# Optimization experiments

Hardware: AMD Instinct MI355X
Metric: run time of the kernel (lower is better)

Reference implementation:

```python
import jax, jax.numpy as jnp
import numpy as np

N_NODES = 200000
N_EDGES = 3200000
N_FEAT = 8
DT_INIT = 0.3
DT_MIN, DT_MAX = 0.02, 2.0
CG_MAX_ITER = 30
CG_TOL = 1e-4
G_INIT = 9.81


def setup_inputs() -> dict:
    key = jax.random.key(0)
    k1, k2, k3, k4 = jax.random.split(key, 4)
    u_now = jax.random.normal(k1, (N_NODES, N_FEAT), dtype=jnp.float32)
    # DAG edges: src < dst (required by the module's topo-level build)
    a = jax.random.randint(k2, (N_EDGES,), 0, N_NODES)
    b = jax.random.randint(k3, (N_EDGES,), 0, N_NODES)
    src = jnp.minimum(a, b)
    dst = jnp.maximum(a, b)
    dst = jnp.where(src == dst, jnp.minimum(dst + 1, N_NODES - 1), dst)
    src = jnp.where(src == dst, jnp.maximum(src - 1, 0), src)
    edge_index = jnp.stack([src, dst]).astype(jnp.int64)
    # edge_attr[:,0]=dx (positive), edge_attr[:,1]=dz
    edge_attr = jax.random.uniform(k4, (N_EDGES, 2), dtype=jnp.float32,
                                   minval=0.05, maxval=1.0)
    dt = jnp.asarray(DT_INIT, dtype=jnp.float32)
    g_hat = jnp.asarray(G_INIT, dtype=jnp.float32)
    return {"u_now": u_now, "edge_index": edge_index, "edge_attr": edge_attr,
            "dt": dt, "g_hat": g_hat}


def _cg_solve(mv, rhs, max_iter, tol):
    # matches torch cg_solve with x0=None (zeros)
    x = jnp.zeros_like(rhs)
    r = rhs - mv(x)
    p = r
    rs = jnp.sum(r * r)

    def body(i, state):
        x, r, p, rs, done = state
        Ap = mv(p)
        alpha = rs / (jnp.sum(p * Ap) + 1e-12)
        x1 = x + alpha * p
        r1 = r - alpha * Ap
        rs1 = jnp.sum(r1 * r1)
        done1 = done | (jnp.sqrt(rs1) <= tol)
        beta = rs1 / (rs + 1e-12)
        p1 = r1 + beta * p
        sel = lambda old, new: jnp.where(done, old, new)
        return (sel(x, x1), sel(r, r1), sel(p, p1),
                jnp.where(done, rs, rs1), done1)

    x, _, _, _, _ = jax.lax.fori_loop(
        0, max_iter, body, (x, r, p, rs, jnp.array(False)))
    return x


def reference(u_now, edge_index, edge_attr, dt, g_hat):
    src, dst = edge_index[0], edge_index[1]
    E = src.shape[0]
    F = u_now.shape[1]
    dx = jnp.clip(edge_attr[:, 0], 1e-6, None)        # [E]
    inv = (1.0 / dx)[:, None]                         # [E,1]
    slope_e = (edge_attr[:, 1] / dx)[:, None]         # [E,1] dz/dx
    dt_eff = jnp.clip(dt, DT_MIN, DT_MAX)

    def D1(x):  # upwind: out[i] += (x[i]-x[j])*inv_dx
        return jnp.zeros_like(x).at[dst].add((x[dst] - x[src]) * inv)

    def D1_T(y):
        yd = y[dst] * inv
        return jnp.zeros_like(y).at[dst].add(yd).at[src].add(-yd)

    A_mv = lambda v: v + dt_eff * (u_now * D1(v))
    AT_mv = lambda y: y + dt_eff * D1_T(u_now * y)

    # slope source term scattered to dst nodes
    slope_n = jnp.zeros_like(u_now).at[dst].add(
        jnp.broadcast_to(slope_e, (E, F)))
    b = u_now - dt_eff * g_hat * slope_n

    # necg: solve (A^T A) x = A^T b via CG
    rhs = AT_mv(b)
    mv = lambda v: AT_mv(A_mv(v))
    u_next = _cg_solve(mv, rhs, CG_MAX_ITER, CG_TOL)
    return u_next
```

## Files before the change

kernel.cpp:

```cpp
#include <hip/hip_runtime.h>
#include <math.h>
#include <stdint.h>
#include <string.h>


#define F 8
#define CG_ITERS 30
#define LEAF_T 4096
#define LEAF_PAD (LEAF_T + LEAF_T / 128 + 8)
#define ENC_ADD 1024
#define MAX_LEAF 1024
#define MAX_CLS 32


#define LV(A_, i_) A_[(i_) + ((i_) >> 7)]

struct __align__(8) Ed { int n; float v; };
struct __align__(16) Rec { int e; int n; float v; float s; };

struct Sched {
    int NL, uNT, uMaxD, nCls;
    int leafOff[MAX_LEAF], leafN[MAX_LEAF], cls[MAX_LEAF];
    int cNB[MAX_CLS], cMaxD[MAX_CLS];
    int cBOff[MAX_CLS][64], cBN[MAX_CLS][64];
    int cA[MAX_CLS][64], cB[MAX_CLS][64], cOrder[MAX_CLS][64];
    int cLevOff[MAX_CLS][32];
    int uA[MAX_LEAF], uB[MAX_LEAF], uOrder[MAX_LEAF], uLevOff[64];
};


static void host_build_tree(int n, int T, int* bOff, int* bN,
                            int* A, int* B, int* dep,
                            int* pNB, int* pNT, int* pMaxD) {
    int so[64], sn[64], st[64], sid[64], sdp[64];
    int sp = 0, coff = 0, cn = n, c2 = 0, t = 0, rootd = 0;
    for (;;) {
        if (cn <= T) {
            if (bOff) { bOff[c2] = coff; bN[c2] = cn; }
            int id = c2, dp = 0; c2++;
            bool fin = false;
            for (;;) {
                if (sp == 0) { rootd = dp; fin = true; break; }
                if (st[sp - 1] == 0) {
                    st[sp - 1] = 1; sid[sp - 1] = id; sdp[sp - 1] = dp;
                    int n2 = sn[sp - 1] / 2; n2 -= (n2 & 7);
                    coff = so[sp - 1] + n2; cn = sn[sp - 1] - n2;
                    break;
                } else {
                    A[t] = sid[sp - 1]; B[t] = id;
                    int dA = sdp[sp - 1];
                    dp = ((dA > dp) ? dA : dp) + 1;
                    dep[t] = dp;
                    id = ENC_ADD + t; t++;
                    sp--;
                }
            }
            if (fin) break;
        } else {
            so[sp] = coff; sn[sp] = cn; st[sp] = 0; sp++;
            int n2 = cn / 2; n2 -= (n2 & 7);
            cn = n2;
        }
    }
    *pNB = c2; *pNT = t; *pMaxD = rootd;
}

static void host_bucketize(const int* dep, int NT, int maxD,
                           int* order, int* levOff) {
    int cnt[64];
    for (int d = 0; d <= maxD; ++d) cnt[d] = 0;
    for (int t = 0; t < NT; ++t) cnt[dep[t]]++;
    int run = 0;
    levOff[0] = 0;
    for (int d = 1; d <= maxD; ++d) { run += cnt[d]; levOff[d] = run; }
    int cur[64];
    for (int d = 1; d <= maxD; ++d) cur[d] = levOff[d - 1];
    for (int t = 0; t < NT; ++t) { int d = dep[t]; order[cur[d]++] = t; }
}

static void build_sched_host(int n, Sched* s) {
    static int uDep[MAX_LEAF];
    host_build_tree(n, LEAF_T, s->leafOff, s->leafN, s->uA, s->uB, uDep,
                    &s->NL, &s->uNT, &s->uMaxD);
    host_bucketize(uDep, s->uNT, s->uMaxD, s->uOrder, s->uLevOff);
    s->nCls = 0;
    int clsN[MAX_CLS];
    int dep[64];
    for (int j = 0; j < s->NL; ++j) {
        int c = -1;
        for (int k = 0; k < s->nCls; ++k)
            if (clsN[k] == s->leafN[j]) { c = k; break; }
        if (c < 0 && s->nCls < MAX_CLS) {
            c = s->nCls++;
            clsN[c] = s->leafN[j];
            int NB, NT, maxD;
            host_build_tree(s->leafN[j], 128, s->cBOff[c], s->cBN[c],
                            s->cA[c], s->cB[c], dep, &NB, &NT, &maxD);
            s->cNB[c] = NB; s->cMaxD[c] = maxD;
            host_bucketize(dep, NT, maxD, s->cOrder[c], s->cLevOff[c]);
        }
        s->cls[j] = c;
    }
}


__device__ __forceinline__ float dt_eff_of(const float* dtp) {
    return fminf(fmaxf(dtp[0], 0.02f), 2.0f);
}

__device__ __forceinline__ int slotOf(int e, int NB) {
    return (e < ENC_ADD) ? e : (NB + (e - ENC_ADD));
}

__device__ __forceinline__ float combine_upper(const float* __restrict__ partial,
                                               const Sched* __restrict__ sc,
                                               float* sU, int lane) {
    int NL = sc->NL, NT = sc->uNT, maxD = sc->uMaxD;
    for (int k = lane; k < NL; k += 256) sU[k] = partial[k];
    __syncthreads();
    for (int d = 1; d <= maxD; ++d) {
        int s0 = sc->uLevOff[d - 1], s1 = sc->uLevOff[d];
        for (int s = s0 + lane; s < s1; s += 256) {
            int tt = sc->uOrder[s];
            sU[NL + tt] = __fadd_rn(sU[slotOf(sc->uA[tt], NL)],
                                    sU[slotOf(sc->uB[tt], NL)]);
        }
        __syncthreads();
    }
    return (NT > 0) ? sU[NL + NT - 1] : sU[0];
}

__device__ __forceinline__ void dot_eval(const float* sA, const float* sB,
                                         float* sChain, float* sVal,
                                         int lane, int NB,
                                         const int* __restrict__ bOff,
                                         const int* __restrict__ bN,
                                         const int* __restrict__ A,
                                         const int* __restrict__ Bb,
                                         const int* __restrict__ order,
                                         const int* __restrict__ levOff,
                                         int maxD,
                                         float* __restrict__ partial, int j) {
    int bb = lane >> 3, jj = lane & 7;
    if (bb < NB) {
        int off = bOff[bb], n = bN[bb];
        if (n >= 8) {
            int lim = n - (n & 7);
            float rr = __fmul_rn(LV(sA, off + jj), LV(sB, off + jj));
            for (int e = jj + 8; e < lim; e += 8)
                rr = __fadd_rn(rr, __fmul_rn(LV(sA, off + e), LV(sB, off + e)));
            sChain[bb * 8 + jj] = rr;
        }
    }
    __syncthreads();
    if (lane < NB) {
        int off = bOff[lane], n = bN[lane];
        float res;
        if (n < 8) {
            res = 0.f;
            for (int e = 0; e < n; ++e)
                res = __fadd_rn(res, __fmul_rn(LV(sA, off + e), LV(sB, off + e)));
        } else {
            int lim = n - (n & 7);
            const float* c = sChain + lane * 8;
            res = __fadd_rn(__fadd_rn(__fadd_rn(c[0], c[1]), __fadd_rn(c[2], c[3])),
                            __fadd_rn(__fadd_rn(c[4], c[5]), __fadd_rn(c[6], c[7])));
            for (int e = lim; e < n; ++e)
                res = __fadd_rn(res, __fmul_rn(LV(sA, off + e), LV(sB, off + e)));
        }
        sVal[lane] = res;
    }
    __syncthreads();
    for (int d = 1; d <= maxD; ++d) {
        int s0 = levOff[d - 1], s1 = levOff[d];
        for (int s = s0 + lane; s < s1; s += 256) {
            int tt = order[s];
            sVal[NB + tt] = __fadd_rn(sVal[slotOf(A[tt], NB)],
                                      sVal[slotOf(Bb[tt], NB)]);
        }
        __syncthreads();
    }
    if (lane == 0) partial[j] = (NB > 1) ? sVal[NB + NB - 2] : sVal[0];
}

__global__ void k_dot_leaf(const float* __restrict__ a, const float* __restrict__ b,
                           const Sched* __restrict__ sc, float* __restrict__ partial) {
    __shared__ float sA[LEAF_PAD], sB[LEAF_PAD];
    __shared__ float sChain[512];
    __shared__ float sVal[160];
    int j = blockIdx.x, lane = threadIdx.x;
    int P = sc->leafOff[j] + 1, nn = sc->leafN[j];
    for (int g = lane; g < nn; g += 256) {
        float av = a[P + g], bv = b[P + g];
        int m = g + (g >> 7);
        sA[m] = av; sB[m] = bv;
    }
    __syncthreads();
    int c = sc->cls[j];
    dot_eval(sA, sB, sChain, sVal, lane, sc->cNB[c], sc->cBOff[c], sc->cBN[c],
             sc->cA[c], sc->cB[c], sc->cOrder[c], sc->cLevOff[c], sc->cMaxD[c],
             partial, j);
}

__global__ void k_dot_rs0(const float* __restrict__ a,
                          const float* __restrict__ partial,
                          const Sched* __restrict__ sc, float* __restrict__ scal) {
    __shared__ float sU[2048];
    int lane = threadIdx.x;
    float res = combine_upper(partial, sc, sU, lane);
    if (lane == 0)
        scal[8 + 0] = __fadd_rn(__fmul_rn(a[0], a[0]), res);
}

__global__ void k_xr_dot(float* __restrict__ x, float* __restrict__ r,
                         const float* __restrict__ p, const float* __restrict__ z,
                         const float* __restrict__ scal,
                         const Sched* __restrict__ sc,
                         const float* __restrict__ partial1,
                         float* __restrict__ partial2, int it) {
    __shared__ float sA[LEAF_PAD];
    __shared__ float sU[2048];
    __shared__ float sChain[512];
    __shared__ float sVal[160];
    __shared__ float sAl;
    __shared__ int   sAct;
    int j = blockIdx.x, lane = threadIdx.x;
    float res = combine_upper(partial1, sc, sU, lane);
    if (lane == 0) {
        float pt = __fadd_rn(__fmul_rn(p[0], z[0]), res);
        sAl = __fdiv_rn(scal[8 + it], __fadd_rn(pt, (float)1e-12));
        sAct = (scal[64 + it] == 0.f) ? 1 : 0;
    }
    __syncthreads();
    int active = sAct;
    float al = sAl;
    int P = sc->leafOff[j] + 1, nn = sc->leafN[j];
    if (j == 0 && lane == 0 && active) {
        x[0] = __fadd_rn(x[0], __fmul_rn(al, p[0]));
        r[0] = __fsub_rn(r[0], __fmul_rn(al, z[0]));
    }
    for (int g = lane; g < nn; g += 256) {
        int q = P + g;
        float rv = r[q];
        if (active) {
            float xv = x[q], pv = p[q], zv = z[q];
            x[q] = __fadd_rn(xv, __fmul_rn(al, pv));
            rv = __fsub_rn(rv, __fmul_rn(al, zv));
            r[q] = rv;
        }
        sA[g + (g >> 7)] = rv;
    }
    __syncthreads();
    int c = sc->cls[j];
    dot_eval(sA, sA, sChain, sVal, lane, sc->cNB[c], sc->cBOff[c], sc->cBN[c],
             sc->cA[c], sc->cB[c], sc->cOrder[c], sc->cLevOff[c], sc->cMaxD[c],
             partial2, j);
}

__global__ void k_p_fin(float4* __restrict__ p4, const float4* __restrict__ r4,
                        const float* __restrict__ rfull,
                        float* __restrict__ scal,
                        const Sched* __restrict__ sc,
                        const float* __restrict__ partial2, int it, int n4) {
    __shared__ float sU[2048];
    __shared__ float sBe;
    __shared__ int   sAct;
    int lane = threadIdx.x;
    float res = combine_upper(partial2, sc, sU, lane);
    if (lane == 0) {
        float rs1 = __fadd_rn(__fmul_rn(rfull[0], rfull[0]), res);
        float RS = scal[8 + it];
        float dn = scal[64 + it];
        sBe = __fdiv_rn(rs1, __fadd_rn(RS, (float)1e-12));
        sAct = (dn == 0.f) ? 1 : 0;
        if (blockIdx.x == 0) {
            scal[8 + it + 1]  = (dn == 0.f) ? rs1 : RS;
            scal[64 + it + 1] = (dn != 0.f || __fsqrt_rn(rs1) <= (float)1e-4)
                                ? 1.f : 0.f;
        }
    }
    __syncthreads();
    if (!sAct) return;
    float be = sBe;
    int i = blockIdx.x * blockDim.x + lane;
    if (i >= n4) return;
    float4 pv = p4[i], rv = r4[i];
    pv.x = __fadd_rn(rv.x, __fmul_rn(be, pv.x));
    pv.y = __fadd_rn(rv.y, __fmul_rn(be, pv.y));
    pv.z = __fadd_rn(rv.z, __fmul_rn(be, pv.z));
    pv.w = __fadd_rn(rv.w, __fmul_rn(be, pv.w));
    p4[i] = pv;
}


__global__ void k_edge_pre(const int* __restrict__ dst, const int* __restrict__ src,
                           int* __restrict__ dstCnt, int* __restrict__ srcCnt, int E) {
    int e = blockIdx.x * blockDim.x + threadIdx.x;
    if (e >= E) return;
    atomicAdd(&dstCnt[dst[e]], 1);
    atomicAdd(&srcCnt[src[e]], 1);
}

__global__ void k_scan1(const int* __restrict__ cnt, int* __restrict__ incl,
                        int* __restrict__ bsums, int N) {
    __shared__ int sm[512];
    int i = blockIdx.x * 512 + threadIdx.x;
    sm[threadIdx.x] = (i < N) ? cnt[i] : 0;
    __syncthreads();
    for (int off = 1; off < 512; off <<= 1) {
        int t = (threadIdx.x >= off) ? sm[threadIdx.x - off] : 0;
        __syncthreads();
        sm[threadIdx.x] += t;
        __syncthreads();
    }
    if (i < N) incl[i] = sm[threadIdx.x];
    if (threadIdx.x == 511) bsums[blockIdx.x] = sm[511];
}

__global__ void k_scan2(int* __restrict__ bsums, int nb) {
    __shared__ int sm[512];
    sm[threadIdx.x] = (threadIdx.x < nb) ? bsums[threadIdx.x] : 0;
    __syncthreads();
    for (int off = 1; off < 512; off <<= 1) {
        int t = (threadIdx.x >= off) ? sm[threadIdx.x - off] : 0;
        __syncthreads();
        sm[threadIdx.x] += t;
        __syncthreads();
    }
    if (threadIdx.x < nb) bsums[threadIdx.x] = sm[threadIdx.x];
}

__global__ void k_scan3(int* __restrict__ off, const int* __restrict__ bsums,
                        const int* __restrict__ cnt, int N, int E) {
    int i = blockIdx.x * 512 + threadIdx.x;
    if (i < N) {
        int add = (blockIdx.x > 0) ? bsums[blockIdx.x - 1] : 0;
        off[i] = off[i] + add - cnt[i];
    }
    if (i == 0) off[N] = E;
}

__global__ void k_fill(const int* __restrict__ dst, const int* __restrict__ src,
                       const float* __restrict__ ea,
                       const int* __restrict__ dstOff, const int* __restrict__ srcOff,
                       int* __restrict__ cursD, int* __restrict__ cursS,
                       Rec* __restrict__ recD, Rec* __restrict__ recS, int E) {
    int e = blockIdx.x * blockDim.x + threadIdx.x;
    if (e >= E) return;
    int d = dst[e];
    int s0 = src[e];
    float2 exy = ((const float2*)ea)[e];
    float dx = fmaxf(exy.x, 1e-6f);
    float iv = __fdiv_rn(1.f, dx);
    float sl = __fdiv_rn(exy.y, dx);
    Rec rd; rd.e = e; rd.n = s0; rd.v = iv; rd.s = sl;
    Rec rs; rs.e = e; rs.n = d;  rs.v = iv; rs.s = 0.f;
    recD[dstOff[d] + atomicAdd(&cursD[d], 1)] = rd;
    recS[srcOff[s0] + atomicAdd(&cursS[s0], 1)] = rs;
}

__device__ __forceinline__ void insortR(Rec* L, int lo, int hi) {
    for (int a = lo + 1; a < hi; ++a) {
        Rec key = L[a]; int b = a - 1;
        while (b >= lo && L[b].e > key.e) { L[b + 1] = L[b]; b--; }
        L[b + 1] = key;
    }
}

__global__ void k_sort(const int* __restrict__ dstOff, const int* __restrict__ srcOff,
                       Rec* __restrict__ recD, Rec* __restrict__ recS, int N) {
    int i = blockIdx.x * blockDim.x + threadIdx.x;
    if (i >= N) return;
    insortR(recD, dstOff[i], dstOff[i + 1]);
    insortR(recS, srcOff[i], srcOff[i + 1]);
}

__global__ void k_compact(const Rec* __restrict__ recD, const Rec* __restrict__ recS,
                          Ed* __restrict__ edD, float* __restrict__ slopeD,
                          Ed* __restrict__ edS, int E) {
    int k = blockIdx.x * blockDim.x + threadIdx.x;
    if (k >= E) return;
    Rec rd = recD[k];
    Rec rs = recS[k];
    Ed d0; d0.n = rd.n; d0.v = rd.v;
    Ed s0; s0.n = rs.n; s0.v = rs.v;
    edD[k] = d0;
    edS[k] = s0;
    slopeD[k] = rd.s;
}


__global__ void k_slope_b(const float* __restrict__ u, const float* __restrict__ slopeD,
                          const int* __restrict__ dstOff,
                          float* __restrict__ r, float* __restrict__ y,
                          const float* __restrict__ dtp, const float* __restrict__ gp,
                          int N) {
    int i = blockIdx.x * blockDim.x + threadIdx.x;
    if (i >= N) return;
    float dtg = __fmul_rn(dt_eff_of(dtp), gp[0]);
    float sn = 0.f;
    int k0 = dstOff[i], k1 = dstOff[i + 1];
    for (int k = k0; k < k1; ++k) sn = __fadd_rn(sn, slopeD[k]);
    float ms = __fmul_rn(dtg, sn);
    const float4* u4 = (const float4*)u;
    float4* r4 = (float4*)r;
    float4* y4 = (float4*)y;
    #pragma unroll
    for (int hh = 0; hh < 2; ++hh) {
        float4 uv = u4[i * 2 + hh];
        float4 bv;
        bv.x = __fsub_rn(uv.x, ms);
        bv.y = __fsub_rn(uv.y, ms);
        bv.z = __fsub_rn(uv.z, ms);
        bv.w = __fsub_rn(uv.w, ms);
        r4[i * 2 + hh] = bv;
        float4 yv;
        yv.x = __fmul_rn(uv.x, bv.x);
        yv.y = __fmul_rn(uv.y, bv.y);
        yv.z = __fmul_rn(uv.z, bv.z);
        yv.w = __fmul_rn(uv.w, bv.w);
        y4[i * 2 + hh] = yv;
    }
}

__global__ void k_d1tz_full(const Ed* __restrict__ edD, const int* __restrict__ dstOff,
                            const Ed* __restrict__ edS, const int* __restrict__ srcOff,
                            const float* __restrict__ y,
                            const float* __restrict__ base, float* __restrict__ out,
                            const float* __restrict__ dtp,
                            float* __restrict__ rInit, float* __restrict__ xInit,
                            int NP) {
    int idx = blockIdx.x * blockDim.x + threadIdx.x;
    if (idx >= NP) return;
    int i = idx >> 2, c = idx & 3;
    const float2* y2 = (const float2*)y;
    float2 uy = y2[idx];
    float2 acc = make_float2(0.f, 0.f);
    int k0 = dstOff[i], k1 = dstOff[i + 1];
    #pragma unroll 4
    for (int k = k0; k < k1; ++k) {
        float iv = edD[k].v;
        acc.x = __fadd_rn(acc.x, __fmul_rn(uy.x, iv));
        acc.y = __fadd_rn(acc.y, __fmul_rn(uy.y, iv));
    }
    k0 = srcOff[i]; k1 = srcOff[i + 1];
    #pragma unroll 4
    for (int k = k0; k < k1; ++k) {
        Ed e = edS[k];
        float2 yd = y2[e.n * 4 + c];
        float t0 = __fmul_rn(yd.x, e.v); acc.x = __fadd_rn(acc.x, -t0);
        float t1 = __fmul_rn(yd.y, e.v); acc.y = __fadd_rn(acc.y, -t1);
    }
    float dt = dt_eff_of(dtp);
    float2 bs = ((const float2*)base)[idx];
    float2 ov;
    ov.x = __fadd_rn(bs.x, __fmul_rn(dt, acc.x));
    ov.y = __fadd_rn(bs.y, __fmul_rn(dt, acc.y));
    ((float2*)out)[idx] = ov;
    ((float2*)rInit)[idx] = ov;
    ((float2*)xInit)[idx] = make_float2(0.f, 0.f);
}

__global__ void k_d1w_f(const Ed* __restrict__ edD, const int* __restrict__ dstOff,
                        const float* __restrict__ pv, const float* __restrict__ u,
                        float* __restrict__ w, float* __restrict__ y,
                        float* __restrict__ dacc,
                        const float* __restrict__ dtp, int NP) {
    int idx = blockIdx.x * blockDim.x + threadIdx.x;
    if (idx >= NP) return;
    int i = idx >> 2, c = idx & 3;
    const float2* pv2 = (const float2*)pv;
    float2 pi = pv2[idx];
    float2 acc = make_float2(0.f, 0.f);
    int k0 = dstOff[i], k1 = dstOff[i + 1];
    #pragma unroll 4
    for (int k = k0; k < k1; ++k) {
        Ed e = edD[k];
        float2 ps = pv2[e.n * 4 + c];
        acc.x = __fadd_rn(acc.x, __fmul_rn(__fsub_rn(pi.x, ps.x), e.v));
        acc.y = __fadd_rn(acc.y, __fmul_rn(__fsub_rn(pi.y, ps.y), e.v));
    }
    float dt = dt_eff_of(dtp);
    float2 uv = ((const float2*)u)[idx];
    float2 wv;
    wv.x = __fadd_rn(pi.x, __fmul_rn(dt, __fmul_rn(uv.x, acc.x)));
    wv.y = __fadd_rn(pi.y, __fmul_rn(dt, __fmul_rn(uv.y, acc.y)));
    ((float2*)w)[idx] = wv;
    float2 yv;
    yv.x = __fmul_rn(uv.x, wv.x);
    yv.y = __fmul_rn(uv.y, wv.y);
    ((float2*)y)[idx] = yv;
    float2 da = make_float2(0.f, 0.f);
    #pragma unroll 4
    for (int k = k0; k < k1; ++k) {
        float iv = edD[k].v;
        da.x = __fadd_rn(da.x, __fmul_rn(yv.x, iv));
        da.y = __fadd_rn(da.y, __fmul_rn(yv.y, iv));
    }
    ((float2*)dacc)[idx] = da;
}

__global__ void k_d1tzs(const Ed* __restrict__ edS, const int* __restrict__ srcOff,
                        const float* __restrict__ y, const float* __restrict__ dacc,
                        const float* __restrict__ base, float* __restrict__ out,
                        const float* __restrict__ dtp, int NP) {
    int idx = blockIdx.x * blockDim.x + threadIdx.x;
    if (idx >= NP) return;
    int i = idx >> 2, c = idx & 3;
    const float2* y2 = (const float2*)y;
    float2 acc = ((const float2*)dacc)[idx];
    int k0 = srcOff[i], k1 = srcOff[i + 1];
    #pragma unroll 4
    for (int k = k0; k < k1; ++k) {
        Ed e = edS[k];
        float2 yd = y2[e.n * 4 + c];
        float t0 = __fmul_rn(yd.x, e.v); acc.x = __fadd_rn(acc.x, -t0);
        float t1 = __fmul_rn(yd.y, e.v); acc.y = __fadd_rn(acc.y, -t1);
    }
    float dt = dt_eff_of(dtp);
    float2 bs = ((const float2*)base)[idx];
    float2 ov;
    ov.x = __fadd_rn(bs.x, __fmul_rn(dt, acc.x));
    ov.y = __fadd_rn(bs.y, __fmul_rn(dt, acc.y));
    ((float2*)out)[idx] = ov;
}

extern "C" void kernel_launch(void* const* d_in, const int* in_sizes, int n_in,
                              void* d_out, int out_size, void* d_ws, size_t ws_size,
                              hipStream_t stream) {
    const float* u   = (const float*)d_in[0];
    const int*   ei  = (const int*)d_in[1];
    const float* ea  = (const float*)d_in[2];
    const float* dtp = (const float*)d_in[3];
    const float* gp  = (const float*)d_in[4];

    const int NF = in_sizes[0];
    const int N  = NF / F;
    const int E  = in_sizes[2] / 2;
    const int* srcp = ei;
    const int* dstp = ei + E;

    static Sched h_sched;
    build_sched_host(NF - 1, &h_sched);
    const int NL = h_sched.NL;

    char* wp = (char*)d_ws;
    float* scal    = (float*)wp; wp += 128 * 4;
    float* r       = (float*)wp; wp += (size_t)NF * 4;
    float* p       = (float*)wp; wp += (size_t)NF * 4;
    float* t       = (float*)wp; wp += (size_t)NF * 4;
    float* w       = (float*)wp; wp += (size_t)NF * 4;
    float* y       = (float*)wp; wp += (size_t)NF * 4;
    float* dacc    = (float*)wp; wp += (size_t)NF * 4;
    Rec*   recD    = (Rec*)wp;   wp += (size_t)E * 16;
    Rec*   recS    = (Rec*)wp;   wp += (size_t)E * 16;
    Ed*    edD     = (Ed*)wp;    wp += (size_t)E * 8;
    Ed*    edS     = (Ed*)wp;    wp += (size_t)E * 8;
    float* slopeD  = (float*)wp; wp += (size_t)E * 4;
    int*   dstOff  = (int*)wp;   wp += (size_t)(N + 1) * 4;
    int*   srcOff  = (int*)wp;   wp += (size_t)(N + 1) * 4;
    int*   dstCnt  = (int*)wp;   wp += (size_t)N * 4;
    int*   srcCnt  = (int*)wp;   wp += (size_t)N * 4;
    int*   cursD   = (int*)wp;   wp += (size_t)N * 4;
    int*   cursS   = (int*)wp;   wp += (size_t)N * 4;
    int*   bsD     = (int*)wp;   wp += 512 * 4;
    int*   bsS     = (int*)wp;   wp += 512 * 4;
    float* partial1 = (float*)wp; wp += 2048 * 4;
    float* partial2 = (float*)wp; wp += 2048 * 4;
    wp = (char*)(((uintptr_t)wp + 255) & ~(uintptr_t)255);
    Sched* d_sched = (Sched*)wp; wp += (sizeof(Sched) + 255) & ~(size_t)255;
    float* x = (float*)d_out;

    hipMemcpyAsync(d_sched, &h_sched, sizeof(Sched), hipMemcpyHostToDevice,
                   stream);
    hipMemsetAsync(scal, 0, 128 * 4, stream);
    hipMemsetAsync(dstCnt, 0, (size_t)N * 4, stream);
    hipMemsetAsync(srcCnt, 0, (size_t)N * 4, stream);
    hipMemsetAsync(cursD, 0, (size_t)N * 4, stream);
    hipMemsetAsync(cursS, 0, (size_t)N * 4, stream);

    const int bn = 256;
    const int gN  = (N + bn - 1) / bn;
    const int gE  = (E + bn - 1) / bn;
    const int nb  = (N + 511) / 512;
    const int n4  = NF / 4;
    const int g4  = (n4 + bn - 1) / bn;
    const int NP  = NF / 2;
    const int gP  = (NP + bn - 1) / bn;

    k_edge_pre<<<gE, bn, 0, stream>>>(dstp, srcp, dstCnt, srcCnt, E);
    k_scan1<<<nb, 512, 0, stream>>>(dstCnt, dstOff, bsD, N);
    k_scan2<<<1, 512, 0, stream>>>(bsD, nb);
    k_scan3<<<nb, 512, 0, stream>>>(dstOff, bsD, dstCnt, N, E);
    k_scan1<<<nb, 512, 0, stream>>>(srcCnt, srcOff, bsS, N);
    k_scan2<<<1, 512, 0, stream>>>(bsS, nb);
    k_scan3<<<nb, 512, 0, stream>>>(srcOff, bsS, srcCnt, N, E);
    k_fill<<<gE, bn, 0, stream>>>(dstp, srcp, ea, dstOff, srcOff, cursD, cursS,
                                  recD, recS, E);
    k_sort<<<gN, bn, 0, stream>>>(dstOff, srcOff, recD, recS, N);
    k_compact<<<gE, bn, 0, stream>>>(recD, recS, edD, slopeD, edS, E);

    k_slope_b<<<gN, bn, 0, stream>>>(u, slopeD, dstOff, r, y, dtp, gp, N);
    k_d1tz_full<<<gP, bn, 0, stream>>>(edD, dstOff, edS, srcOff,
                                       y, r, p, dtp, r, x, NP);
    k_dot_leaf<<<NL, 256, 0, stream>>>(p, p, d_sched, partial1);
    k_dot_rs0<<<1, 256, 0, stream>>>(p, partial1, d_sched, scal);

    for (int it = 0; it < CG_ITERS; ++it) {
        k_d1w_f<<<gP, bn, 0, stream>>>(edD, dstOff, p, u, w, y, dacc, dtp, NP);
        k_d1tzs<<<gP, bn, 0, stream>>>(edS, srcOff, y, dacc, w, t, dtp, NP);
        k_dot_leaf<<<NL, 256, 0, stream>>>(p, t, d_sched, partial1);
        k_xr_dot<<<NL, 256, 0, stream>>>(x, r, p, t, scal, d_sched,
                                         partial1, partial2, it);
        k_p_fin<<<g4, bn, 0, stream>>>((float4*)p, (const float4*)r, r, scal,
                                       d_sched, partial2, it, n4);
    }
}
```

Measured before the change: 4.662 ms.

## Fuse CSR scans, merge sort+compact with shared-memory key sort, merge memsets

Merges the dst and src prefix-scan kernels into combined launches, replaces the in-place global-memory insertion sort plus separate compact pass with a single kernel that sorts packed (edge id, local index) keys in shared memory and writes compacted edge arrays directly, and collapses four memsets into one contiguous memset. This is meant to cut launch count and the global-memory traffic of sorting 16-byte records in place. Shared memory of 64 KB per block may limit occupancy, and nodes with degree above 64 fall back to a quadratic selection scan. The single memset relies on dstCnt, srcCnt, cursD and cursS being contiguous in the workspace.

After: 4.568 ms. -2.0%, faster.

```diff
diff --git a/kernel.cpp b/kernel.cpp
--- a/kernel.cpp
+++ b/kernel.cpp
@@ -11,6 +11,7 @@
 #define ENC_ADD 1024
 #define MAX_LEAF 1024
 #define MAX_CLS 32
+#define MAXDEG 64
 
 
 #define LV(A_, i_) A_[(i_) + ((i_) >> 7)]
@@ -301,10 +302,18 @@
     atomicAdd(&srcCnt[src[e]], 1);
 }
 
-__global__ void k_scan1(const int* __restrict__ cnt, int* __restrict__ incl,
-                        int* __restrict__ bsums, int N) {
+__global__ void k_scan1m(const int* __restrict__ cntD, const int* __restrict__ cntS,
+                         int* __restrict__ inclD, int* __restrict__ inclS,
+                         int* __restrict__ bsD, int* __restrict__ bsS,
+                         int N, int nb) {
     __shared__ int sm[512];
-    int i = blockIdx.x * 512 + threadIdx.x;
+    int bb = blockIdx.x;
+    int isS = (bb >= nb) ? 1 : 0;
+    int blk = bb - (isS ? nb : 0);
+    const int* cnt = isS ? cntS : cntD;
+    int* incl = isS ? inclS : inclD;
+    int* bsums = isS ? bsS : bsD;
+    int i = blk * 512 + threadIdx.x;
     sm[threadIdx.x] = (i < N) ? cnt[i] : 0;
     __syncthreads();
     for (int off = 1; off < 512; off <<= 1) {
@@ -314,27 +323,39 @@
         __syncthreads();
     }
     if (i < N) incl[i] = sm[threadIdx.x];
-    if (threadIdx.x == 511) bsums[blockIdx.x] = sm[511];
-}
-
-__global__ void k_scan2(int* __restrict__ bsums, int nb) {
+    if (threadIdx.x == 511) bsums[blk] = sm[511];
+}
+
+__global__ void k_scan2m(int* __restrict__ bsD, int* __restrict__ bsS, int nb) {
     __shared__ int sm[512];
-    sm[threadIdx.x] = (threadIdx.x < nb) ? bsums[threadIdx.x] : 0;
-    __syncthreads();
-    for (int off = 1; off < 512; off <<= 1) {
-        int t = (threadIdx.x >= off) ? sm[threadIdx.x - off] : 0;
+    for (int pass = 0; pass < 2; ++pass) {
+        int* bsums = pass ? bsS : bsD;
+        sm[threadIdx.x] = (threadIdx.x < nb) ? bsums[threadIdx.x] : 0;
         __syncthreads();
-        sm[threadIdx.x] += t;
+        for (int off = 1; off < 512; off <<= 1) {
+            int t = (threadIdx.x >= off) ? sm[threadIdx.x - off] : 0;
+            __syncthreads();
+            sm[threadIdx.x] += t;
+            __syncthreads();
+        }
+        if (threadIdx.x < nb) bsums[threadIdx.x] = sm[threadIdx.x];
         __syncthreads();
     }
-    if (threadIdx.x < nb) bsums[threadIdx.x] = sm[threadIdx.x];
-}
-
-__global__ void k_scan3(int* __restrict__ off, const int* __restrict__ bsums,
-                        const int* __restrict__ cnt, int N, int E) {
-    int i = blockIdx.x * 512 + threadIdx.x;
+}
+
+__global__ void k_scan3m(int* __restrict__ offD, int* __restrict__ offS,
+                         const int* __restrict__ bsD, const int* __restrict__ bsS,
+                         const int* __restrict__ cntD, const int* __restrict__ cntS,
+                         int N, int E, int nb) {
+    int bb = blockIdx.x;
+    int isS = (bb >= nb) ? 1 : 0;
+    int blk = bb - (isS ? nb : 0);
+    int* off = isS ? offS : offD;
+    const int* bsums = isS ? bsS : bsD;
+    const int* cnt = isS ? cntS : cntD;
+    int i = blk * 512 + threadIdx.x;
     if (i < N) {
-        int add = (blockIdx.x > 0) ? bsums[blockIdx.x - 1] : 0;
+        int add = (blk > 0) ? bsums[blk - 1] : 0;
         off[i] = off[i] + add - cnt[i];
     }
     if (i == 0) off[N] = E;
@@ -359,34 +380,74 @@
     recS[srcOff[s0] + atomicAdd(&cursS[s0], 1)] = rs;
 }
 
-__device__ __forceinline__ void insortR(Rec* L, int lo, int hi) {
-    for (int a = lo + 1; a < hi; ++a) {
-        Rec key = L[a]; int b = a - 1;
-        while (b >= lo && L[b].e > key.e) { L[b + 1] = L[b]; b--; }
-        L[b + 1] = key;
-    }
-}
-
-__global__ void k_sort(const int* __restrict__ dstOff, const int* __restrict__ srcOff,
-                       Rec* __restrict__ recD, Rec* __restrict__ recS, int N) {
+__global__ void k_sortc(const int* __restrict__ dstOff, const int* __restrict__ srcOff,
+                        const Rec* __restrict__ recD, const Rec* __restrict__ recS,
+                        Ed* __restrict__ edD, float* __restrict__ slopeD,
+                        Ed* __restrict__ edS, int N) {
+    __shared__ unsigned keys[256 * MAXDEG];
     int i = blockIdx.x * blockDim.x + threadIdx.x;
     if (i >= N) return;
-    insortR(recD, dstOff[i], dstOff[i + 1]);
-    insortR(recS, srcOff[i], srcOff[i + 1]);
-}
-
-__global__ void k_compact(const Rec* __restrict__ recD, const Rec* __restrict__ recS,
-                          Ed* __restrict__ edD, float* __restrict__ slopeD,
-                          Ed* __restrict__ edS, int E) {
-    int k = blockIdx.x * blockDim.x + threadIdx.x;
-    if (k >= E) return;
-    Rec rd = recD[k];
-    Rec rs = recS[k];
-    Ed d0; d0.n = rd.n; d0.v = rd.v;
-    Ed s0; s0.n = rs.n; s0.v = rs.v;
-    edD[k] = d0;
-    edS[k] = s0;
-    slopeD[k] = rd.s;
+    unsigned* k0 = keys + threadIdx.x * MAXDEG;
+    {
+        int lo = dstOff[i], hi = dstOff[i + 1], d = hi - lo;
+        if (d <= MAXDEG) {
+            for (int m = 0; m < d; ++m)
+                k0[m] = ((unsigned)recD[lo + m].e << 6) | (unsigned)m;
+            for (int a = 1; a < d; ++a) {
+                unsigned kk = k0[a]; int b = a - 1;
+                while (b >= 0 && k0[b] > kk) { k0[b + 1] = k0[b]; b--; }
+                k0[b + 1] = kk;
+            }
+            for (int m = 0; m < d; ++m) {
+                Rec rr = recD[lo + (int)(k0[m] & 63u)];
+                Ed ed; ed.n = rr.n; ed.v = rr.v;
+                edD[lo + m] = ed; slopeD[lo + m] = rr.s;
+            }
+        } else {
+            int prev = -1;
+            for (int m = 0; m < d; ++m) {
+                int best = 0x7fffffff, bj = -1;
+                for (int jx = 0; jx < d; ++jx) {
+                    int ev = recD[lo + jx].e;
+                    if (ev > prev && ev < best) { best = ev; bj = jx; }
+                }
+                Rec rr = recD[lo + bj];
+                Ed ed; ed.n = rr.n; ed.v = rr.v;
+                edD[lo + m] = ed; slopeD[lo + m] = rr.s;
+                prev = best;
+            }
+        }
+    }
+    {
+        int lo = srcOff[i], hi = srcOff[i + 1], d = hi - lo;
+        if (d <= MAXDEG) {
+            for (int m = 0; m < d; ++m)
+                k0[m] = ((unsigned)recS[lo + m].e << 6) | (unsigned)m;
+            for (int a = 1; a < d; ++a) {
+                unsigned kk = k0[a]; int b = a - 1;
+                while (b >= 0 && k0[b] > kk) { k0[b + 1] = k0[b]; b--; }
+                k0[b + 1] = kk;
+            }
+            for (int m = 0; m < d; ++m) {
+                Rec rr = recS[lo + (int)(k0[m] & 63u)];
+                Ed ed; ed.n = rr.n; ed.v = rr.v;
+                edS[lo + m] = ed;
+            }
+        } else {
+            int prev = -1;
+            for (int m = 0; m < d; ++m) {
+                int best = 0x7fffffff, bj = -1;
+                for (int jx = 0; jx < d; ++jx) {
+                    int ev = recS[lo + jx].e;
+                    if (ev > prev && ev < best) { best = ev; bj = jx; }
+                }
+                Rec rr = recS[lo + bj];
+                Ed ed; ed.n = rr.n; ed.v = rr.v;
+                edS[lo + m] = ed;
+                prev = best;
+            }
+        }
+    }
 }
 
 
@@ -574,10 +635,7 @@
     hipMemcpyAsync(d_sched, &h_sched, sizeof(Sched), hipMemcpyHostToDevice,
                    stream);
     hipMemsetAsync(scal, 0, 128 * 4, stream);
-    hipMemsetAsync(dstCnt, 0, (size_t)N * 4, stream);
-    hipMemsetAsync(srcCnt, 0, (size_t)N * 4, stream);
-    hipMemsetAsync(cursD, 0, (size_t)N * 4, stream);
-    hipMemsetAsync(cursS, 0, (size_t)N * 4, stream);
+    hipMemsetAsync(dstCnt, 0, (size_t)N * 4 * 4, stream);
 
     const int bn = 256;
     const int gN  = (N + bn - 1) / bn;
@@ -589,16 +647,15 @@
     const int gP  = (NP + bn - 1) / bn;
 
     k_edge_pre<<<gE, bn, 0, stream>>>(dstp, srcp, dstCnt, srcCnt, E);
-    k_scan1<<<nb, 512, 0, stream>>>(dstCnt, dstOff, bsD, N);
-    k_scan2<<<1, 512, 0, stream>>>(bsD, nb);
-    k_scan3<<<nb, 512, 0, stream>>>(dstOff, bsD, dstCnt, N, E);
-    k_scan1<<<nb, 512, 0, stream>>>(srcCnt, srcOff, bsS, N);
-    k_scan2<<<1, 512, 0, stream>>>(bsS, nb);
-    k_scan3<<<nb, 512, 0, stream>>>(srcOff, bsS, srcCnt, N, E);
+    k_scan1m<<<2 * nb, 512, 0, stream>>>(dstCnt, srcCnt, dstOff, srcOff,
+                                         bsD, bsS, N, nb);
+    k_scan2m<<<1, 512, 0, stream>>>(bsD, bsS, nb);
+    k_scan3m<<<2 * nb, 512, 0, stream>>>(dstOff, srcOff, bsD, bsS,
+                                         dstCnt, srcCnt, N, E, nb);
     k_fill<<<gE, bn, 0, stream>>>(dstp, srcp, ea, dstOff, srcOff, cursD, cursS,
                                   recD, recS, E);
-    k_sort<<<gN, bn, 0, stream>>>(dstOff, srcOff, recD, recS, N);
-    k_compact<<<gE, bn, 0, stream>>>(recD, recS, edD, slopeD, edS, E);
+    k_sortc<<<gN, bn, 0, stream>>>(dstOff, srcOff, recD, recS,
+                                   edD, slopeD, edS, N);
 
     k_slope_b<<<gN, bn, 0, stream>>>(u, slopeD, dstOff, r, y, dtp, gp, N);
     k_d1tz_full<<<gP, bn, 0, stream>>>(edD, dstOff, edS, srcOff,
```
